# Kernel tuning notes

Measured on AMD Instinct MI355X. Metric: run time of the kernel, lower is better.

## Reference

```python
import jax, jax.numpy as jnp
import numpy as np

SEQ, B, IN, H = 512, 64, 1024, 1024

def _lstm_layer(x_seq, Wx, bx, Wh, bh):
    # x_seq: [S, B, D], Wx: [4H, D], Wh: [4H, H]
    h0 = jnp.zeros((x_seq.shape[1], Wh.shape[1]), x_seq.dtype)
    c0 = jnp.zeros_like(h0)
    def step(carry, x_t):
        h, c = carry
        z = x_t @ Wx.T + bx + h @ Wh.T + bh  # [B, 4H]
        i, f, g, o = jnp.split(z, 4, axis=1)
        c1 = jax.nn.sigmoid(f) * c + jax.nn.sigmoid(i) * jnp.tanh(g)
        h1 = jax.nn.sigmoid(o) * jnp.tanh(c1)
        return (h1, c1), h1
    _, hs = jax.lax.scan(step, (h0, c0), x_seq)
    return hs  # [S, B, H]

def setup_inputs() -> dict:
    key = jax.random.key(0)
    ks = jax.random.split(key, 9)
    s_in = 1.0 / np.sqrt(IN)
    s_h = 1.0 / np.sqrt(H)
    return {
        "x": jax.random.normal(ks[0], (SEQ, B, IN), jnp.float32),
        "Wx0": jax.random.uniform(ks[1], (4 * H, IN), jnp.float32, -s_in, s_in),
        "bx0": jax.random.uniform(ks[2], (4 * H,), jnp.float32, -s_in, s_in),
        "Wh0": jax.random.uniform(ks[3], (4 * H, H), jnp.float32, -s_h, s_h),
        "bh0": jax.random.uniform(ks[4], (4 * H,), jnp.float32, -s_h, s_h),
        "Wx1": jax.random.uniform(ks[5], (4 * H, H), jnp.float32, -s_h, s_h),
        "bx1": jax.random.uniform(ks[6], (4 * H,), jnp.float32, -s_h, s_h),
        "Wh1": jax.random.uniform(ks[7], (4 * H, H), jnp.float32, -s_h, s_h),
        "bh1": jax.random.uniform(ks[8], (4 * H,), jnp.float32, -s_h, s_h),
    }

def reference(x, Wx0, bx0, Wh0, bh0, Wx1, bx1, Wh1, bh1):
    # Two stacked unidirectional LSTM layers, zero initial states.
    h_seq0 = _lstm_layer(x, Wx0, bx0, Wh0, bh0)
    h_seq1 = _lstm_layer(h_seq0, Wx1, bx1, Wh1, bh1)
    return h_seq1  # [S, B, H] = stacked version of the torch list output
```

## Files before the change

kernel.cpp:

```cpp
#include <hip/hip_runtime.h>


#define SEQ   512
#define BATCH 64
#define HID   1024
#define NG    4096
#define KCAT  2048
#define F0_BASE 0
#define E0_IDX  8192
#define F1_BASE 16384
#define E1_IDX  24576

#define SMEM_BYTES 133504

typedef __attribute__((ext_vector_type(8))) _Float16 f16x8;
typedef __attribute__((ext_vector_type(4))) _Float16 f16x4;
typedef __attribute__((ext_vector_type(4))) float    f32x4;

__device__ __forceinline__ float sigm_f(float x){ return 1.f/(1.f + __expf(-x)); }
__device__ __forceinline__ float tanh_f(float x){
    float e = __expf(-2.f*fabsf(x));
    float r = (1.f - e)/(1.f + e);
    return copysignf(r, x);
}

__device__ __forceinline__ void store_h8(_Float16* p, f16x4 v){
    asm volatile("global_store_dwordx2 %0, %1, off sc0 sc1" :: "v"(p), "v"(v) : "memory");
}
__device__ __forceinline__ void drain_vmem(){
    asm volatile("s_waitcnt vmcnt(0)" ::: "memory");
}


__global__ void prep_w_kernel(const float* __restrict__ Wx, const float* __restrict__ Wh,
                              const float* __restrict__ bx, const float* __restrict__ bh,
                              _Float16* __restrict__ Wr, float* __restrict__ br){
    int p = blockIdx.x;
    int j = p >> 2, g = p & 3;
    int r = g*1024 + j;
    int k = threadIdx.x * 8;
    const float* s = (k < 1024) ? (Wx + (size_t)r*1024 + k)
                                : (Wh + (size_t)r*1024 + (k - 1024));
    float4 v0 = *reinterpret_cast<const float4*>(s);
    float4 v1 = *reinterpret_cast<const float4*>(s + 4);
    f16x8 o;
    o[0]=(_Float16)v0.x; o[1]=(_Float16)v0.y; o[2]=(_Float16)v0.z; o[3]=(_Float16)v0.w;
    o[4]=(_Float16)v1.x; o[5]=(_Float16)v1.y; o[6]=(_Float16)v1.z; o[7]=(_Float16)v1.w;
    *reinterpret_cast<f16x8*>(Wr + (size_t)p*KCAT + k) = o;
    if (threadIdx.x == 0) br[p] = bx[r] + bh[r];
}

__global__ void prep_x_kernel(const float* __restrict__ x, _Float16* xo){
    size_t i = ((size_t)blockIdx.x*256 + threadIdx.x) * 8;
    float4 v0 = *reinterpret_cast<const float4*>(x + i);
    float4 v1 = *reinterpret_cast<const float4*>(x + i + 4);
    f16x8 o;
    o[0]=(_Float16)v0.x; o[1]=(_Float16)v0.y; o[2]=(_Float16)v0.z; o[3]=(_Float16)v0.w;
    o[4]=(_Float16)v1.x; o[5]=(_Float16)v1.y; o[6]=(_Float16)v1.z; o[7]=(_Float16)v1.w;
    *reinterpret_cast<f16x8*>(xo + i) = o;
}

__global__ void init_misc_kernel(int* flags, _Float16* hz){
    int i = blockIdx.x*256 + threadIdx.x;
    flags[i] = 0;
    if (i < 16384){
        f16x4 z; z[0]=(_Float16)0.f; z[1]=(_Float16)0.f; z[2]=(_Float16)0.f; z[3]=(_Float16)0.f;
        *reinterpret_cast<f16x4*>(hz + (size_t)i*4) = z;
    }
}


__device__ __forceinline__ void wait_epoch_g(const int* flags, int eidx, int k, int rep){
    for(;;){
        int e = __hip_atomic_load(&flags[eidx + rep*32], __ATOMIC_RELAXED, __HIP_MEMORY_SCOPE_AGENT);
        if (e >= k) break;
        __builtin_amdgcn_s_sleep(2);
    }
    asm volatile("" ::: "memory");
}

__device__ __forceinline__ void aggregate_publish(int* flags, int base, int eidx,
                                                  int k, int lane){
    const int b = lane*4;
    for(;;){
        int a0 = __hip_atomic_load(&flags[base + (b+0)*32], __ATOMIC_RELAXED, __HIP_MEMORY_SCOPE_AGENT);
        int a1 = __hip_atomic_load(&flags[base + (b+1)*32], __ATOMIC_RELAXED, __HIP_MEMORY_SCOPE_AGENT);
        int a2 = __hip_atomic_load(&flags[base + (b+2)*32], __ATOMIC_RELAXED, __HIP_MEMORY_SCOPE_AGENT);
        int a3 = __hip_atomic_load(&flags[base + (b+3)*32], __ATOMIC_RELAXED, __HIP_MEMORY_SCOPE_AGENT);
        bool ok = (a0>=k) && (a1>=k) && (a2>=k) && (a3>=k);
        if (__all(ok)) break;
        __builtin_amdgcn_s_sleep(1);
    }
    asm volatile("" ::: "memory");
    if (lane < 32)
        __hip_atomic_store(&flags[eidx + lane*32], k, __ATOMIC_RELAXED, __HIP_MEMORY_SCOPE_AGENT);
}


__device__ __forceinline__ f32x4 mfma16(f16x8 a, f16x8 b, f32x4 c){
    return __builtin_amdgcn_mfma_f32_16x16x32_f16(a, b, c, 0, 0, 0);
}

__device__ __forceinline__ void gemm_half_ldsb(const _Float16* A, const char* wrow,
                                               int c0, int swz, f32x4* acc){
    f16x8 a[32];
    #pragma unroll
    for (int kk = 0; kk < 8; ++kk)
        #pragma unroll
        for (int m = 0; m < 4; ++m)
            a[kk*4+m] = *reinterpret_cast<const f16x8*>(A + kk*32 + m*16*1024);
    #pragma unroll
    for (int kk = 0; kk < 8; ++kk){
        f16x8 bb = *reinterpret_cast<const f16x8*>(wrow + ((c0 + kk*64) ^ swz));
        acc[0] = mfma16(a[kk*4+0], bb, acc[0]);
        acc[1] = mfma16(a[kk*4+1], bb, acc[1]);
        acc[2] = mfma16(a[kk*4+2], bb, acc[2]);
        acc[3] = mfma16(a[kk*4+3], bb, acc[3]);
    }
    #pragma unroll
    for (int kk = 8; kk < 16; ++kk)
        #pragma unroll
        for (int m = 0; m < 4; ++m)
            a[(kk-8)*4+m] = *reinterpret_cast<const f16x8*>(A + kk*32 + m*16*1024);
    #pragma unroll
    for (int kk = 8; kk < 16; ++kk){
        f16x8 bb = *reinterpret_cast<const f16x8*>(wrow + ((c0 + kk*64) ^ swz));
        acc[0] = mfma16(a[(kk-8)*4+0], bb, acc[0]);
        acc[1] = mfma16(a[(kk-8)*4+1], bb, acc[1]);
        acc[2] = mfma16(a[(kk-8)*4+2], bb, acc[2]);
        acc[3] = mfma16(a[(kk-8)*4+3], bb, acc[3]);
    }
}

__device__ __forceinline__ void gemm_half_gb(const _Float16* A, const _Float16* Wp,
                                             f32x4* acc){
    f16x8 a[32];
    #pragma unroll
    for (int kk = 0; kk < 8; ++kk)
        #pragma unroll
        for (int m = 0; m < 4; ++m)
            a[kk*4+m] = *reinterpret_cast<const f16x8*>(A + kk*32 + m*16*1024);
    #pragma unroll
    for (int kk = 0; kk < 8; ++kk){
        f16x8 bb = *reinterpret_cast<const f16x8*>(Wp + kk*32);
        acc[0] = mfma16(a[kk*4+0], bb, acc[0]);
        acc[1] = mfma16(a[kk*4+1], bb, acc[1]);
        acc[2] = mfma16(a[kk*4+2], bb, acc[2]);
        acc[3] = mfma16(a[kk*4+3], bb, acc[3]);
    }
    #pragma unroll
    for (int kk = 8; kk < 16; ++kk)
        #pragma unroll
        for (int m = 0; m < 4; ++m)
            a[(kk-8)*4+m] = *reinterpret_cast<const f16x8*>(A + kk*32 + m*16*1024);
    #pragma unroll
    for (int kk = 8; kk < 16; ++kk){
        f16x8 bb = *reinterpret_cast<const f16x8*>(Wp + kk*32);
        acc[0] = mfma16(a[(kk-8)*4+0], bb, acc[0]);
        acc[1] = mfma16(a[(kk-8)*4+1], bb, acc[1]);
        acc[2] = mfma16(a[(kk-8)*4+2], bb, acc[2]);
        acc[3] = mfma16(a[(kk-8)*4+3], bb, acc[3]);
    }
}

__device__ __forceinline__ void gemm_q_f32(const float* A, const _Float16* Wp, f32x4* acc){
    #pragma unroll 2
    for (int kk = 0; kk < 16; ++kk){
        f16x8 b = *reinterpret_cast<const f16x8*>(Wp + kk*32);
        f16x8 a[4];
        #pragma unroll
        for (int m = 0; m < 4; ++m){
            float4 u0 = *reinterpret_cast<const float4*>(A + kk*32 + (size_t)m*16*1024);
            float4 u1 = *reinterpret_cast<const float4*>(A + kk*32 + (size_t)m*16*1024 + 4);
            f16x8 v;
            v[0]=(_Float16)u0.x; v[1]=(_Float16)u0.y; v[2]=(_Float16)u0.z; v[3]=(_Float16)u0.w;
            v[4]=(_Float16)u1.x; v[5]=(_Float16)u1.y; v[6]=(_Float16)u1.z; v[7]=(_Float16)u1.w;
            a[m] = v;
        }
        acc[0] = mfma16(a[0], b, acc[0]);
        acc[1] = mfma16(a[1], b, acc[1]);
        acc[2] = mfma16(a[2], b, acc[2]);
        acc[3] = mfma16(a[3], b, acc[3]);
    }
}


__global__ __launch_bounds__(256, 1)
void lstm_persist(const _Float16* __restrict__ Wr0, const _Float16* __restrict__ Wr1,
                  const float* __restrict__ br0, const float* __restrict__ br1,
                  const _Float16* __restrict__ xbf, const float* __restrict__ xf32,
                  int use_xf16, const _Float16* __restrict__ hz,
                  _Float16* h0ring, _Float16* h1ring, float* out, int* flags){
    extern __shared__ char smem[];
    float (*accL)[4][64][17] = reinterpret_cast<float(*)[4][64][17]>(smem + 98304);

    const int tid  = threadIdx.x;
    const int wg   = blockIdx.x;
    const int wv   = tid >> 6;
    const int lane = tid & 63;
    const int r    = lane & 15;
    const int q    = lane >> 4;
    const int p0   = wg * 16;
    const int rep  = wg & 31;
    const int swz  = (r & 7) << 4;

    for (int idx = tid; idx < 6144; idx += 256){
        int rr, cb; char* dst; const _Float16* s;
        if (idx < 2048){
            rr = idx >> 7;  cb = (idx & 127) << 4;
            s   = Wr0 + (size_t)(p0 + rr)*KCAT + 1024 + (cb >> 1);
            dst = smem + rr*2048 + (cb ^ ((rr & 7) << 4));
        } else {
            int j2 = idx - 2048;
            rr = j2 >> 8;  cb = (j2 & 255) << 4;
            s   = Wr1 + (size_t)(p0 + rr)*KCAT + (cb >> 1);
            dst = smem + 32768 + rr*4096 + (cb ^ ((rr & 7) << 4));
        }
        *reinterpret_cast<f16x8*>(dst) = *reinterpret_cast<const f16x8*>(s);
    }
    __syncthreads();

    f32x4 cst = {0.f,0.f,0.f,0.f};
    f32x4 ho_keep = {0.f,0.f,0.f,0.f};
    f32x4 bias[4];
    {
        const float* bsrc = (wv == 0) ? br0 : br1;
        #pragma unroll
        for (int jj = 0; jj < 4; ++jj)
            bias[jj] = *reinterpret_cast<const f32x4*>(&bsrc[p0 + jj*4]);
    }

    const int kofs = (wv & 1)*512 + q*8;
    const int wcol = wv*512 + q*8;
    const char* w1row  = smem + 32768 + r*4096;
    const char* wh0row = smem + r*2048;
    const size_t BH = (size_t)BATCH*HID;

    for (int k = 0; k <= SEQ; ++k){
        f32x4 acc[4];
        #pragma unroll
        for (int m = 0; m < 4; ++m){ acc[m].x=0;acc[m].y=0;acc[m].z=0;acc[m].w=0; }

        if (wv < 2){
            if (k < SEQ){
                if (use_xf16)
                    gemm_half_gb(xbf + (size_t)k*BH + (size_t)r*HID + kofs,
                                 Wr0 + (size_t)(p0 + r)*KCAT + wcol, acc);
                else
                    gemm_q_f32(xf32 + (size_t)k*BH + (size_t)r*HID + kofs,
                               Wr0 + (size_t)(p0 + r)*KCAT + wcol, acc);
            }
        } else {
            if (k > 0) wait_epoch_g(flags, E0_IDX, k, rep);
            if (k < SEQ){
                const _Float16* A0 = (k == 0) ? (hz + (size_t)r*HID + kofs)
                                              : (h0ring + (size_t)(k-1)*BH + (size_t)r*HID + kofs);
                gemm_half_ldsb(A0, wh0row, (wv-2)*1024 + q*16, swz, acc);
            }
        }

        #pragma unroll
        for (int mt = 0; mt < 4; ++mt)
            #pragma unroll
            for (int j = 0; j < 4; ++j)
                accL[0][wv][mt*16 + q*4 + j][r] = acc[mt][j];
        __syncthreads();

        if (wg == 0 && wv == 3 && k < SEQ)
            aggregate_publish(flags, F0_BASE, E0_IDX, k + 1, lane);

        if (wv == 0 && k < SEQ){
            f32x4 zz[4];
            #pragma unroll
            for (int jj = 0; jj < 4; ++jj) zz[jj] = bias[jj];
            #pragma unroll
            for (int w2 = 0; w2 < 4; ++w2)
                #pragma unroll
                for (int jj = 0; jj < 4; ++jj){
                    f32x4 a = *reinterpret_cast<const f32x4*>(&accL[0][w2][lane][jj*4]);
                    zz[jj].x += a.x; zz[jj].y += a.y; zz[jj].z += a.z; zz[jj].w += a.w;
                }
            f16x4 hv;
            #pragma unroll
            for (int jl = 0; jl < 4; ++jl){
                float ig = sigm_f(zz[jl].x), fg = sigm_f(zz[jl].y);
                float gg = tanh_f(zz[jl].z), og = sigm_f(zz[jl].w);
                float c = fg*cst[jl] + ig*gg;  cst[jl] = c;
                hv[jl] = (_Float16)(og * tanh_f(c));
            }
            store_h8(h0ring + ((size_t)k*BATCH + lane)*HID + wg*4, hv);
            drain_vmem();
            if (lane == 0)
                __hip_atomic_store(&flags[F0_BASE + wg*32], k + 1,
                                   __ATOMIC_RELAXED, __HIP_MEMORY_SCOPE_AGENT);
        }

        #pragma unroll
        for (int m = 0; m < 4; ++m){ acc[m].x=0;acc[m].y=0;acc[m].z=0;acc[m].w=0; }

        if (k >= 1){
            if (wv < 2){
                gemm_half_ldsb(h0ring + (size_t)(k-1)*BH + (size_t)r*HID + kofs,
                               w1row, wv*1024 + q*16, swz, acc);
            } else {
                if (k >= 2) wait_epoch_g(flags, E1_IDX, k-1, rep);
                const _Float16* A1 = (k == 1) ? (hz + (size_t)r*HID + kofs)
                                              : (h1ring + (size_t)(k-2)*BH + (size_t)r*HID + kofs);
                gemm_half_ldsb(A1, w1row, wv*1024 + q*16, swz, acc);
            }
        }

        #pragma unroll
        for (int mt = 0; mt < 4; ++mt)
            #pragma unroll
            for (int j = 0; j < 4; ++j)
                accL[1][wv][mt*16 + q*4 + j][r] = acc[mt][j];
        __syncthreads();

        if (wg == 0 && wv == 2 && k >= 1)
            aggregate_publish(flags, F1_BASE, E1_IDX, k, lane);

        if (wv == 1 && k >= 1){
            const int t1 = k - 1;
            f32x4 zz[4];
            #pragma unroll
            for (int jj = 0; jj < 4; ++jj) zz[jj] = bias[jj];
            #pragma unroll
            for (int w2 = 0; w2 < 4; ++w2)
                #pragma unroll
                for (int jj = 0; jj < 4; ++jj){
                    f32x4 a = *reinterpret_cast<const f32x4*>(&accL[1][w2][lane][jj*4]);
                    zz[jj].x += a.x; zz[jj].y += a.y; zz[jj].z += a.z; zz[jj].w += a.w;
                }
            f16x4 hv; f32x4 ho;
            #pragma unroll
            for (int jl = 0; jl < 4; ++jl){
                float ig = sigm_f(zz[jl].x), fg = sigm_f(zz[jl].y);
                float gg = tanh_f(zz[jl].z), og = sigm_f(zz[jl].w);
                float c = fg*cst[jl] + ig*gg;  cst[jl] = c;
                float h = og * tanh_f(c);
                hv[jl] = (_Float16)h;  ho[jl] = h;
            }
            if (k < SEQ) store_h8(h1ring + ((size_t)t1*BATCH + lane)*HID + wg*4, hv);
            if (t1 < SEQ-1) *reinterpret_cast<f32x4*>(out + ((size_t)t1*BATCH + lane)*HID + wg*4) = ho;
            else            ho_keep = ho;
            drain_vmem();
            if (lane == 0)
                __hip_atomic_store(&flags[F1_BASE + wg*32], k,
                                   __ATOMIC_RELAXED, __HIP_MEMORY_SCOPE_AGENT);
        }
    }

    if (wv == 1){
        wait_epoch_g(flags, E1_IDX, SEQ, rep);
        *reinterpret_cast<f32x4*>(out + ((size_t)(SEQ-1)*BATCH + lane)*HID + wg*4) = ho_keep;
    }
}


extern "C" void kernel_launch(void* const* d_in, const int* in_sizes, int n_in,
                              void* d_out, int out_size, void* d_ws, size_t ws_size,
                              hipStream_t stream){
    const float* x   = (const float*)d_in[0];
    const float* Wx0 = (const float*)d_in[1];
    const float* bx0 = (const float*)d_in[2];
    const float* Wh0 = (const float*)d_in[3];
    const float* bh0 = (const float*)d_in[4];
    const float* Wx1 = (const float*)d_in[5];
    const float* bx1 = (const float*)d_in[6];
    const float* Wh1 = (const float*)d_in[7];
    const float* bh1 = (const float*)d_in[8];
    float* out = (float*)d_out;
    char* ws = (char*)d_ws;

    size_t o = 0;
    _Float16* Wr0 = (_Float16*)(ws + o); o += (size_t)NG*KCAT*2;
    _Float16* Wr1 = (_Float16*)(ws + o); o += (size_t)NG*KCAT*2;
    float* br0 = (float*)(ws + o); o += 16384;
    float* br1 = (float*)(ws + o); o += 16384;
    _Float16* h1ring = (_Float16*)(ws + o); o += (size_t)SEQ*BATCH*HID*2;
    _Float16* hz     = (_Float16*)(ws + o); o += (size_t)BATCH*HID*2;
    int* flags = (int*)(ws + o); o += 131072;

    const size_t RING = (size_t)SEQ*BATCH*HID*2;
    _Float16 *xbf = nullptr, *h0ring;
    int use_xf16 = 0;
    if (ws_size >= o + 2*RING){
        xbf    = (_Float16*)(ws + o);  o += RING;  use_xf16 = 1;
        h0ring = (_Float16*)(ws + o);  o += RING;
    } else if (ws_size >= o + RING){
        xbf    = (_Float16*)(ws + o);  o += RING;  use_xf16 = 1;
        h0ring = (_Float16*)((char*)d_out + (size_t)64*1024*1024);
    } else {
        h0ring = (_Float16*)((char*)d_out + (size_t)64*1024*1024);
    }

    hipFuncSetAttribute((const void*)lstm_persist,
                        hipFuncAttributeMaxDynamicSharedMemorySize, SMEM_BYTES);

    prep_w_kernel<<<NG, 256, 0, stream>>>(Wx0, Wh0, bx0, bh0, Wr0, br0);
    prep_w_kernel<<<NG, 256, 0, stream>>>(Wx1, Wh1, bx1, bh1, Wr1, br1);
    if (use_xf16)
        prep_x_kernel<<<(SEQ*BATCH*HID)/(256*8), 256, 0, stream>>>(x, xbf);
    init_misc_kernel<<<128, 256, 0, stream>>>(flags, hz);
    lstm_persist<<<256, 256, SMEM_BYTES, stream>>>(Wr0, Wr1, br0, br1, xbf, x, use_xf16,
                                                   hz, h0ring, h1ring, out, flags);
}
```

Baseline: 9.370 ms.

## Add dedicated aggregator wave, LDS-counter barriers, and fragment-ordered weight layout

Adds a fifth wave per workgroup. In workgroup 0 it continuously polls all per-block flags and publishes the epoch counters for both layers, replacing the inline aggregate_publish calls that stalled compute waves. The two __syncthreads per step become a monotonic LDS atomic counter barrier over the four compute waves, so the extra aggregator wave can return early. Weights are stored in LDS in MFMA-fragment order, so each lane reads contiguous 16 bytes without XOR swizzle address math. Risks include spin overhead on the LDS counter and the aggregator's polling loop adding memory traffic.

Measured after the change: 11.66 ms. 1.24x slower.

```diff
diff --git a/kernel.cpp b/kernel.cpp
--- a/kernel.cpp
+++ b/kernel.cpp
@@ -11,7 +11,7 @@
 #define F1_BASE 16384
 #define E1_IDX  24576
 
-#define SMEM_BYTES 133504
+#define SMEM_BYTES 133184
 
 typedef __attribute__((ext_vector_type(8))) _Float16 f16x8;
 typedef __attribute__((ext_vector_type(4))) _Float16 f16x4;
@@ -70,30 +70,36 @@
 }
 
 
+__device__ __forceinline__ int gload(const int* p){
+    return __hip_atomic_load(p, __ATOMIC_RELAXED, __HIP_MEMORY_SCOPE_AGENT);
+}
+__device__ __forceinline__ void gstore(int* p, int v){
+    __hip_atomic_store(p, v, __ATOMIC_RELAXED, __HIP_MEMORY_SCOPE_AGENT);
+}
+
 __device__ __forceinline__ void wait_epoch_g(const int* flags, int eidx, int k, int rep){
     for(;;){
-        int e = __hip_atomic_load(&flags[eidx + rep*32], __ATOMIC_RELAXED, __HIP_MEMORY_SCOPE_AGENT);
+        int e = gload(&flags[eidx + rep*32]);
         if (e >= k) break;
         __builtin_amdgcn_s_sleep(2);
     }
     asm volatile("" ::: "memory");
 }
 
-__device__ __forceinline__ void aggregate_publish(int* flags, int base, int eidx,
-                                                  int k, int lane){
-    const int b = lane*4;
-    for(;;){
-        int a0 = __hip_atomic_load(&flags[base + (b+0)*32], __ATOMIC_RELAXED, __HIP_MEMORY_SCOPE_AGENT);
-        int a1 = __hip_atomic_load(&flags[base + (b+1)*32], __ATOMIC_RELAXED, __HIP_MEMORY_SCOPE_AGENT);
-        int a2 = __hip_atomic_load(&flags[base + (b+2)*32], __ATOMIC_RELAXED, __HIP_MEMORY_SCOPE_AGENT);
-        int a3 = __hip_atomic_load(&flags[base + (b+3)*32], __ATOMIC_RELAXED, __HIP_MEMORY_SCOPE_AGENT);
-        bool ok = (a0>=k) && (a1>=k) && (a2>=k) && (a3>=k);
-        if (__all(ok)) break;
+__device__ __forceinline__ int wave_min(int v){
+    #pragma unroll
+    for (int off = 1; off < 64; off <<= 1)
+        v = min(v, __shfl_xor(v, off));
+    return v;
+}
+
+__device__ __forceinline__ void bar4(int* cnt, int target){
+    asm volatile("s_waitcnt lgkmcnt(0)" ::: "memory");
+    if ((threadIdx.x & 63) == 0)
+        __hip_atomic_fetch_add(cnt, 1, __ATOMIC_RELAXED, __HIP_MEMORY_SCOPE_WORKGROUP);
+    while (__hip_atomic_load(cnt, __ATOMIC_RELAXED, __HIP_MEMORY_SCOPE_WORKGROUP) < target)
         __builtin_amdgcn_s_sleep(1);
-    }
     asm volatile("" ::: "memory");
-    if (lane < 32)
-        __hip_atomic_store(&flags[eidx + lane*32], k, __ATOMIC_RELAXED, __HIP_MEMORY_SCOPE_AGENT);
 }
 
 
@@ -101,8 +107,8 @@
     return __builtin_amdgcn_mfma_f32_16x16x32_f16(a, b, c, 0, 0, 0);
 }
 
-__device__ __forceinline__ void gemm_half_ldsb(const _Float16* A, const char* wrow,
-                                               int c0, int swz, f32x4* acc){
+__device__ __forceinline__ void gemm_half_ldsb(const _Float16* A, const char* wfrag,
+                                               f32x4* acc){
     f16x8 a[32];
     #pragma unroll
     for (int kk = 0; kk < 8; ++kk)
@@ -111,7 +117,7 @@
             a[kk*4+m] = *reinterpret_cast<const f16x8*>(A + kk*32 + m*16*1024);
     #pragma unroll
     for (int kk = 0; kk < 8; ++kk){
-        f16x8 bb = *reinterpret_cast<const f16x8*>(wrow + ((c0 + kk*64) ^ swz));
+        f16x8 bb = *reinterpret_cast<const f16x8*>(wfrag + kk*1024);
         acc[0] = mfma16(a[kk*4+0], bb, acc[0]);
         acc[1] = mfma16(a[kk*4+1], bb, acc[1]);
         acc[2] = mfma16(a[kk*4+2], bb, acc[2]);
@@ -124,7 +130,7 @@
             a[(kk-8)*4+m] = *reinterpret_cast<const f16x8*>(A + kk*32 + m*16*1024);
     #pragma unroll
     for (int kk = 8; kk < 16; ++kk){
-        f16x8 bb = *reinterpret_cast<const f16x8*>(wrow + ((c0 + kk*64) ^ swz));
+        f16x8 bb = *reinterpret_cast<const f16x8*>(wfrag + kk*1024);
         acc[0] = mfma16(a[(kk-8)*4+0], bb, acc[0]);
         acc[1] = mfma16(a[(kk-8)*4+1], bb, acc[1]);
         acc[2] = mfma16(a[(kk-8)*4+2], bb, acc[2]);
@@ -185,7 +191,7 @@
 }
 
 
-__global__ __launch_bounds__(256, 1)
+__global__ __launch_bounds__(320, 1)
 void lstm_persist(const _Float16* __restrict__ Wr0, const _Float16* __restrict__ Wr1,
                   const float* __restrict__ br0, const float* __restrict__ br1,
                   const _Float16* __restrict__ xbf, const float* __restrict__ xf32,
@@ -193,6 +199,7 @@
                   _Float16* h0ring, _Float16* h1ring, float* out, int* flags){
     extern __shared__ char smem[];
     float (*accL)[4][64][17] = reinterpret_cast<float(*)[4][64][17]>(smem + 98304);
+    int* barCnt = reinterpret_cast<int*>(smem + 133120);
 
     const int tid  = threadIdx.x;
     const int wg   = blockIdx.x;
@@ -202,23 +209,50 @@
     const int q    = lane >> 4;
     const int p0   = wg * 16;
     const int rep  = wg & 31;
-    const int swz  = (r & 7) << 4;
-
-    for (int idx = tid; idx < 6144; idx += 256){
-        int rr, cb; char* dst; const _Float16* s;
+
+    for (int idx = tid; idx < 6144; idx += 320){
+        const _Float16* s; char* dst;
         if (idx < 2048){
-            rr = idx >> 7;  cb = (idx & 127) << 4;
-            s   = Wr0 + (size_t)(p0 + rr)*KCAT + 1024 + (cb >> 1);
-            dst = smem + rr*2048 + (cb ^ ((rr & 7) << 4));
+            int wvh = idx >> 10, kk = (idx >> 6) & 15, ln = idx & 63;
+            s = Wr0 + (size_t)(p0 + (ln & 15))*KCAT + 1024 + wvh*512 + kk*32 + (ln >> 4)*8;
+            dst = smem + idx*16;
         } else {
-            int j2 = idx - 2048;
-            rr = j2 >> 8;  cb = (j2 & 255) << 4;
-            s   = Wr1 + (size_t)(p0 + rr)*KCAT + (cb >> 1);
-            dst = smem + 32768 + rr*4096 + (cb ^ ((rr & 7) << 4));
+            int d = idx - 2048;
+            int wvd = d >> 10, kk = (d >> 6) & 15, ln = d & 63;
+            s = Wr1 + (size_t)(p0 + (ln & 15))*KCAT + wvd*512 + kk*32 + (ln >> 4)*8;
+            dst = smem + 32768 + d*16;
         }
         *reinterpret_cast<f16x8*>(dst) = *reinterpret_cast<const f16x8*>(s);
     }
+    if (tid == 0) *barCnt = 0;
     __syncthreads();
+
+    if (wv == 4){
+        if (wg == 0){
+            int e0 = 0, e1 = 0;
+            for(;;){
+                int f0 = 0x7fffffff, f1 = 0x7fffffff;
+                #pragma unroll
+                for (int j = 0; j < 4; ++j){
+                    int i4 = lane*4 + j;
+                    f0 = min(f0, gload(&flags[F0_BASE + i4*32]));
+                    f1 = min(f1, gload(&flags[F1_BASE + i4*32]));
+                }
+                int g0 = wave_min(f0), g1 = wave_min(f1);
+                if (g0 > e0){
+                    if (lane < 32) gstore(&flags[E0_IDX + lane*32], g0);
+                    e0 = g0;
+                }
+                if (g1 > e1){
+                    if (lane < 32) gstore(&flags[E1_IDX + lane*32], g1);
+                    e1 = g1;
+                }
+                if (e1 >= SEQ) break;
+                __builtin_amdgcn_s_sleep(1);
+            }
+        }
+        return;
+    }
 
     f32x4 cst = {0.f,0.f,0.f,0.f};
     f32x4 ho_keep = {0.f,0.f,0.f,0.f};
@@ -232,9 +266,10 @@
 
     const int kofs = (wv & 1)*512 + q*8;
     const int wcol = wv*512 + q*8;
-    const char* w1row  = smem + 32768 + r*4096;
-    const char* wh0row = smem + r*2048;
+    const char* wh0frag = smem + (wv >= 2 ? (wv-2)*16384 : 0) + lane*16;
+    const char* w1frag  = smem + 32768 + wv*16384 + lane*16;
     const size_t BH = (size_t)BATCH*HID;
+    int btgt = 4;
 
     for (int k = 0; k <= SEQ; ++k){
         f32x4 acc[4];
@@ -255,7 +290,7 @@
             if (k < SEQ){
                 const _Float16* A0 = (k == 0) ? (hz + (size_t)r*HID + kofs)
                                               : (h0ring + (size_t)(k-1)*BH + (size_t)r*HID + kofs);
-                gemm_half_ldsb(A0, wh0row, (wv-2)*1024 + q*16, swz, acc);
+                gemm_half_ldsb(A0, wh0frag, acc);
             }
         }
 
@@ -264,10 +299,7 @@
             #pragma unroll
             for (int j = 0; j < 4; ++j)
                 accL[0][wv][mt*16 + q*4 + j][r] = acc[mt][j];
-        __syncthreads();
-
-        if (wg == 0 && wv == 3 && k < SEQ)
-            aggregate_publish(flags, F0_BASE, E0_IDX, k + 1, lane);
+        bar4(barCnt, btgt); btgt += 4;
 
         if (wv == 0 && k < SEQ){
             f32x4 zz[4];
@@ -290,9 +322,7 @@
             }
             store_h8(h0ring + ((size_t)k*BATCH + lane)*HID + wg*4, hv);
             drain_vmem();
-            if (lane == 0)
-                __hip_atomic_store(&flags[F0_BASE + wg*32], k + 1,
-                                   __ATOMIC_RELAXED, __HIP_MEMORY_SCOPE_AGENT);
+            if (lane == 0) gstore(&flags[F0_BASE + wg*32], k + 1);
         }
 
         #pragma unroll
@@ -301,12 +331,12 @@
         if (k >= 1){
             if (wv < 2){
                 gemm_half_ldsb(h0ring + (size_t)(k-1)*BH + (size_t)r*HID + kofs,
-                               w1row, wv*1024 + q*16, swz, acc);
+                               w1frag, acc);
             } else {
                 if (k >= 2) wait_epoch_g(flags, E1_IDX, k-1, rep);
                 const _Float16* A1 = (k == 1) ? (hz + (size_t)r*HID + kofs)
                                               : (h1ring + (size_t)(k-2)*BH + (size_t)r*HID + kofs);
-                gemm_half_ldsb(A1, w1row, wv*1024 + q*16, swz, acc);
+                gemm_half_ldsb(A1, w1frag, acc);
             }
         }
 
@@ -315,10 +345,7 @@
             #pragma unroll
             for (int j = 0; j < 4; ++j)
                 accL[1][wv][mt*16 + q*4 + j][r] = acc[mt][j];
-        __syncthreads();
-
-        if (wg == 0 && wv == 2 && k >= 1)
-            aggregate_publish(flags, F1_BASE, E1_IDX, k, lane);
+        bar4(barCnt, btgt); btgt += 4;
 
         if (wv == 1 && k >= 1){
             const int t1 = k - 1;
@@ -345,9 +372,7 @@
             if (t1 < SEQ-1) *reinterpret_cast<f32x4*>(out + ((size_t)t1*BATCH + lane)*HID + wg*4) = ho;
             else            ho_keep = ho;
             drain_vmem();
-            if (lane == 0)
-                __hip_atomic_store(&flags[F1_BASE + wg*32], k,
-                                   __ATOMIC_RELAXED, __HIP_MEMORY_SCOPE_AGENT);
+            if (lane == 0) gstore(&flags[F1_BASE + wg*32], k);
         }
     }
 
@@ -403,6 +428,6 @@
     if (use_xf16)
         prep_x_kernel<<<(SEQ*BATCH*HID)/(256*8), 256, 0, stream>>>(x, xbf);
     init_misc_kernel<<<128, 256, 0, stream>>>(flags, hz);
-    lstm_persist<<<256, 256, SMEM_BYTES, stream>>>(Wr0, Wr1, br0, br1, xbf, x, use_xf16,
+    lstm_persist<<<256, 320, SMEM_BYTES, stream>>>(Wr0, Wr1, br0, br1, xbf, x, use_xf16,
                                                    hz, h0ring, h1ring, out, flags);
 }
```

## Issue GEMM operand loads in inline asm batches, pre-fragment LDS weights, move aggregation into waiters

Applied to the files above, without the earlier changes.

The two GEMM helpers are rewritten to issue every global A and B fragment load up front through inline-asm global_load_dwordx4 with fixed offsets, separated by sched_barriers and a single vmcnt wait, so the loads overlap instead of being spread out by the compiler. The recurrent weights are stored in LDS in per-lane fragment order, which removes the XOR swizzle address math. The aggregate_publish step for each epoch now runs inside the waiting warp of workgroup 0, in place of its wait_epoch_g call, rather than after a __syncthreads, which shortens the path to the global barrier. A final epoch flag is added so the last output store stays correctly synchronised. The risks are higher register pressure from holding 32 to 40 vector loads at once, and subtle correctness problems in the reworked barrier protocol.

Result: faster. 8.766 ms (median of 2 runs) (-6.5%).

```diff
diff --git a/kernel.cpp b/kernel.cpp
--- a/kernel.cpp
+++ b/kernel.cpp
@@ -11,7 +11,7 @@
 #define F1_BASE 16384
 #define E1_IDX  24576
 
-#define SMEM_BYTES 133504
+#define SMEM_BYTES 133120
 
 typedef __attribute__((ext_vector_type(8))) _Float16 f16x8;
 typedef __attribute__((ext_vector_type(4))) _Float16 f16x4;
@@ -30,6 +30,19 @@
 __device__ __forceinline__ void drain_vmem(){
     asm volatile("s_waitcnt vmcnt(0)" ::: "memory");
 }
+
+#define GLD(dst, base, OFF) \
+    asm volatile("global_load_dwordx4 %0, %1, off offset:" #OFF \
+                 : "=&v"(dst) : "v"(base))
+#define GLD8L(arr, i, B) \
+    GLD(arr[(i)+0],B,0);   GLD(arr[(i)+1],B,64);  GLD(arr[(i)+2],B,128); GLD(arr[(i)+3],B,192); \
+    GLD(arr[(i)+4],B,256); GLD(arr[(i)+5],B,320); GLD(arr[(i)+6],B,384); GLD(arr[(i)+7],B,448)
+#define GLD8H(arr, i, B) \
+    GLD(arr[(i)+0],B,512); GLD(arr[(i)+1],B,576); GLD(arr[(i)+2],B,640); GLD(arr[(i)+3],B,704); \
+    GLD(arr[(i)+4],B,768); GLD(arr[(i)+5],B,832); GLD(arr[(i)+6],B,896); GLD(arr[(i)+7],B,960)
+#define VMWAIT0 \
+    asm volatile("s_waitcnt vmcnt(0)" ::: "memory"); \
+    __builtin_amdgcn_sched_barrier(0)
 
 
 __global__ void prep_w_kernel(const float* __restrict__ Wx, const float* __restrict__ Wh,
@@ -101,66 +114,68 @@
     return __builtin_amdgcn_mfma_f32_16x16x32_f16(a, b, c, 0, 0, 0);
 }
 
-__device__ __forceinline__ void gemm_half_ldsb(const _Float16* A, const char* wrow,
-                                               int c0, int swz, f32x4* acc){
+__device__ __forceinline__ void gemm_asm_ldsb(const _Float16* A, const char* wfrag,
+                                              f32x4* acc){
+    const _Float16* b0 = A;
+    const _Float16* b1 = A + 16*1024;
+    const _Float16* b2 = A + 32*1024;
+    const _Float16* b3 = A + 48*1024;
     f16x8 a[32];
-    #pragma unroll
-    for (int kk = 0; kk < 8; ++kk)
-        #pragma unroll
-        for (int m = 0; m < 4; ++m)
-            a[kk*4+m] = *reinterpret_cast<const f16x8*>(A + kk*32 + m*16*1024);
+    __builtin_amdgcn_sched_barrier(0);
+    GLD8L(a, 0, b0); GLD8L(a, 8, b1); GLD8L(a, 16, b2); GLD8L(a, 24, b3);
+    VMWAIT0;
     #pragma unroll
     for (int kk = 0; kk < 8; ++kk){
-        f16x8 bb = *reinterpret_cast<const f16x8*>(wrow + ((c0 + kk*64) ^ swz));
-        acc[0] = mfma16(a[kk*4+0], bb, acc[0]);
-        acc[1] = mfma16(a[kk*4+1], bb, acc[1]);
-        acc[2] = mfma16(a[kk*4+2], bb, acc[2]);
-        acc[3] = mfma16(a[kk*4+3], bb, acc[3]);
-    }
-    #pragma unroll
-    for (int kk = 8; kk < 16; ++kk)
-        #pragma unroll
-        for (int m = 0; m < 4; ++m)
-            a[(kk-8)*4+m] = *reinterpret_cast<const f16x8*>(A + kk*32 + m*16*1024);
-    #pragma unroll
-    for (int kk = 8; kk < 16; ++kk){
-        f16x8 bb = *reinterpret_cast<const f16x8*>(wrow + ((c0 + kk*64) ^ swz));
-        acc[0] = mfma16(a[(kk-8)*4+0], bb, acc[0]);
-        acc[1] = mfma16(a[(kk-8)*4+1], bb, acc[1]);
-        acc[2] = mfma16(a[(kk-8)*4+2], bb, acc[2]);
-        acc[3] = mfma16(a[(kk-8)*4+3], bb, acc[3]);
-    }
-}
-
-__device__ __forceinline__ void gemm_half_gb(const _Float16* A, const _Float16* Wp,
-                                             f32x4* acc){
-    f16x8 a[32];
-    #pragma unroll
-    for (int kk = 0; kk < 8; ++kk)
-        #pragma unroll
-        for (int m = 0; m < 4; ++m)
-            a[kk*4+m] = *reinterpret_cast<const f16x8*>(A + kk*32 + m*16*1024);
+        f16x8 bb = *reinterpret_cast<const f16x8*>(wfrag + kk*1024);
+        acc[0] = mfma16(a[kk],      bb, acc[0]);
+        acc[1] = mfma16(a[8 + kk],  bb, acc[1]);
+        acc[2] = mfma16(a[16 + kk], bb, acc[2]);
+        acc[3] = mfma16(a[24 + kk], bb, acc[3]);
+    }
+    __builtin_amdgcn_sched_barrier(0);
+    GLD8H(a, 0, b0); GLD8H(a, 8, b1); GLD8H(a, 16, b2); GLD8H(a, 24, b3);
+    VMWAIT0;
     #pragma unroll
     for (int kk = 0; kk < 8; ++kk){
-        f16x8 bb = *reinterpret_cast<const f16x8*>(Wp + kk*32);
-        acc[0] = mfma16(a[kk*4+0], bb, acc[0]);
-        acc[1] = mfma16(a[kk*4+1], bb, acc[1]);
-        acc[2] = mfma16(a[kk*4+2], bb, acc[2]);
-        acc[3] = mfma16(a[kk*4+3], bb, acc[3]);
-    }
+        f16x8 bb = *reinterpret_cast<const f16x8*>(wfrag + (8 + kk)*1024);
+        acc[0] = mfma16(a[kk],      bb, acc[0]);
+        acc[1] = mfma16(a[8 + kk],  bb, acc[1]);
+        acc[2] = mfma16(a[16 + kk], bb, acc[2]);
+        acc[3] = mfma16(a[24 + kk], bb, acc[3]);
+    }
+    __builtin_amdgcn_sched_barrier(0);
+}
+
+__device__ __forceinline__ void gemm_asm_gb(const _Float16* A, const _Float16* Wp,
+                                            f32x4* acc){
+    const _Float16* b0 = A;
+    const _Float16* b1 = A + 16*1024;
+    const _Float16* b2 = A + 32*1024;
+    const _Float16* b3 = A + 48*1024;
+    f16x8 bw[8], a[32];
+    __builtin_amdgcn_sched_barrier(0);
+    GLD8L(bw, 0, Wp);
+    GLD8L(a, 0, b0); GLD8L(a, 8, b1); GLD8L(a, 16, b2); GLD8L(a, 24, b3);
+    VMWAIT0;
     #pragma unroll
-    for (int kk = 8; kk < 16; ++kk)
-        #pragma unroll
-        for (int m = 0; m < 4; ++m)
-            a[(kk-8)*4+m] = *reinterpret_cast<const f16x8*>(A + kk*32 + m*16*1024);
+    for (int kk = 0; kk < 8; ++kk){
+        acc[0] = mfma16(a[kk],      bw[kk], acc[0]);
+        acc[1] = mfma16(a[8 + kk],  bw[kk], acc[1]);
+        acc[2] = mfma16(a[16 + kk], bw[kk], acc[2]);
+        acc[3] = mfma16(a[24 + kk], bw[kk], acc[3]);
+    }
+    __builtin_amdgcn_sched_barrier(0);
+    GLD8H(bw, 0, Wp);
+    GLD8H(a, 0, b0); GLD8H(a, 8, b1); GLD8H(a, 16, b2); GLD8H(a, 24, b3);
+    VMWAIT0;
     #pragma unroll
-    for (int kk = 8; kk < 16; ++kk){
-        f16x8 bb = *reinterpret_cast<const f16x8*>(Wp + kk*32);
-        acc[0] = mfma16(a[(kk-8)*4+0], bb, acc[0]);
-        acc[1] = mfma16(a[(kk-8)*4+1], bb, acc[1]);
-        acc[2] = mfma16(a[(kk-8)*4+2], bb, acc[2]);
-        acc[3] = mfma16(a[(kk-8)*4+3], bb, acc[3]);
-    }
+    for (int kk = 0; kk < 8; ++kk){
+        acc[0] = mfma16(a[kk],      bw[kk], acc[0]);
+        acc[1] = mfma16(a[8 + kk],  bw[kk], acc[1]);
+        acc[2] = mfma16(a[16 + kk], bw[kk], acc[2]);
+        acc[3] = mfma16(a[24 + kk], bw[kk], acc[3]);
+    }
+    __builtin_amdgcn_sched_barrier(0);
 }
 
 __device__ __forceinline__ void gemm_q_f32(const float* A, const _Float16* Wp, f32x4* acc){
@@ -202,19 +217,18 @@
     const int q    = lane >> 4;
     const int p0   = wg * 16;
     const int rep  = wg & 31;
-    const int swz  = (r & 7) << 4;
 
     for (int idx = tid; idx < 6144; idx += 256){
-        int rr, cb; char* dst; const _Float16* s;
+        const _Float16* s; char* dst;
         if (idx < 2048){
-            rr = idx >> 7;  cb = (idx & 127) << 4;
-            s   = Wr0 + (size_t)(p0 + rr)*KCAT + 1024 + (cb >> 1);
-            dst = smem + rr*2048 + (cb ^ ((rr & 7) << 4));
+            int wvh = idx >> 10, kk = (idx >> 6) & 15, ln = idx & 63;
+            s = Wr0 + (size_t)(p0 + (ln & 15))*KCAT + 1024 + wvh*512 + kk*32 + (ln >> 4)*8;
+            dst = smem + idx*16;
         } else {
-            int j2 = idx - 2048;
-            rr = j2 >> 8;  cb = (j2 & 255) << 4;
-            s   = Wr1 + (size_t)(p0 + rr)*KCAT + (cb >> 1);
-            dst = smem + 32768 + rr*4096 + (cb ^ ((rr & 7) << 4));
+            int d = idx - 2048;
+            int wvd = d >> 10, kk = (d >> 6) & 15, ln = d & 63;
+            s = Wr1 + (size_t)(p0 + (ln & 15))*KCAT + wvd*512 + kk*32 + (ln >> 4)*8;
+            dst = smem + 32768 + d*16;
         }
         *reinterpret_cast<f16x8*>(dst) = *reinterpret_cast<const f16x8*>(s);
     }
@@ -232,8 +246,8 @@
 
     const int kofs = (wv & 1)*512 + q*8;
     const int wcol = wv*512 + q*8;
-    const char* w1row  = smem + 32768 + r*4096;
-    const char* wh0row = smem + r*2048;
+    const char* wh0frag = smem + (wv >= 2 ? (wv-2)*16384 : 0) + lane*16;
+    const char* w1frag  = smem + 32768 + wv*16384 + lane*16;
     const size_t BH = (size_t)BATCH*HID;
 
     for (int k = 0; k <= SEQ; ++k){
@@ -244,18 +258,21 @@
         if (wv < 2){
             if (k < SEQ){
                 if (use_xf16)
-                    gemm_half_gb(xbf + (size_t)k*BH + (size_t)r*HID + kofs,
-                                 Wr0 + (size_t)(p0 + r)*KCAT + wcol, acc);
+                    gemm_asm_gb(xbf + (size_t)k*BH + (size_t)r*HID + kofs,
+                                Wr0 + (size_t)(p0 + r)*KCAT + wcol, acc);
                 else
                     gemm_q_f32(xf32 + (size_t)k*BH + (size_t)r*HID + kofs,
                                Wr0 + (size_t)(p0 + r)*KCAT + wcol, acc);
             }
         } else {
-            if (k > 0) wait_epoch_g(flags, E0_IDX, k, rep);
+            if (k > 0){
+                if (wg == 0 && wv == 3) aggregate_publish(flags, F0_BASE, E0_IDX, k, lane);
+                else                    wait_epoch_g(flags, E0_IDX, k, rep);
+            }
             if (k < SEQ){
                 const _Float16* A0 = (k == 0) ? (hz + (size_t)r*HID + kofs)
                                               : (h0ring + (size_t)(k-1)*BH + (size_t)r*HID + kofs);
-                gemm_half_ldsb(A0, wh0row, (wv-2)*1024 + q*16, swz, acc);
+                gemm_asm_ldsb(A0, wh0frag, acc);
             }
         }
 
@@ -265,9 +282,6 @@
             for (int j = 0; j < 4; ++j)
                 accL[0][wv][mt*16 + q*4 + j][r] = acc[mt][j];
         __syncthreads();
-
-        if (wg == 0 && wv == 3 && k < SEQ)
-            aggregate_publish(flags, F0_BASE, E0_IDX, k + 1, lane);
 
         if (wv == 0 && k < SEQ){
             f32x4 zz[4];
@@ -300,13 +314,16 @@
 
         if (k >= 1){
             if (wv < 2){
-                gemm_half_ldsb(h0ring + (size_t)(k-1)*BH + (size_t)r*HID + kofs,
-                               w1row, wv*1024 + q*16, swz, acc);
+                gemm_asm_ldsb(h0ring + (size_t)(k-1)*BH + (size_t)r*HID + kofs,
+                              w1frag, acc);
             } else {
-                if (k >= 2) wait_epoch_g(flags, E1_IDX, k-1, rep);
+                if (k >= 2){
+                    if (wg == 0 && wv == 2) aggregate_publish(flags, F1_BASE, E1_IDX, k-1, lane);
+                    else                    wait_epoch_g(flags, E1_IDX, k-1, rep);
+                }
                 const _Float16* A1 = (k == 1) ? (hz + (size_t)r*HID + kofs)
                                               : (h1ring + (size_t)(k-2)*BH + (size_t)r*HID + kofs);
-                gemm_half_ldsb(A1, w1row, wv*1024 + q*16, swz, acc);
+                gemm_asm_ldsb(A1, w1frag, acc);
             }
         }
 
@@ -316,9 +333,6 @@
             for (int j = 0; j < 4; ++j)
                 accL[1][wv][mt*16 + q*4 + j][r] = acc[mt][j];
         __syncthreads();
-
-        if (wg == 0 && wv == 2 && k >= 1)
-            aggregate_publish(flags, F1_BASE, E1_IDX, k, lane);
 
         if (wv == 1 && k >= 1){
             const int t1 = k - 1;
@@ -351,8 +365,12 @@
         }
     }
 
+    if (tid == 0)
+        __hip_atomic_store(&flags[F0_BASE + wg*32], SEQ + 1,
+                           __ATOMIC_RELAXED, __HIP_MEMORY_SCOPE_AGENT);
+    if (wg == 0 && wv == 3) aggregate_publish(flags, F0_BASE, E0_IDX, SEQ + 1, lane);
     if (wv == 1){
-        wait_epoch_g(flags, E1_IDX, SEQ, rep);
+        wait_epoch_g(flags, E0_IDX, SEQ + 1, rep);
         *reinterpret_cast<f32x4*>(out + ((size_t)(SEQ-1)*BATCH + lane)*HID + wg*4) = ho_keep;
     }
 }
```
